# Optimization experiments

Hardware: AMD Instinct MI355X
Metric: run time of the kernel (lower is better)

## Reference

```python
import jax, jax.numpy as jnp
import numpy as np

# Standard genetic code, codons ordered by bases A<C<G<T (codon = b1*16 + b2*4 + b3)
GENETIC_CODE = "KNKNTTTTRSRSIIMIQHQHPPPPRRRRLLLLEDEDAAAAGGGGVVVV*Y*YSSSS*CWCLFLF"
V = 66  # codon vocab: 0 = pad, 1 = special, 2..65 = the 64 codons


def _tables():
    uniq = sorted(set(GENETIC_CODE))
    aa2g = {a: i for i, a in enumerate(uniq)}
    g_codon = np.array([aa2g[a] for a in GENETIC_CODE], np.int32)
    n_syn_g = np.bincount(g_codon, minlength=len(uniq))
    group_of_v = np.full(V, len(uniq), np.int32)  # pad/special -> dummy group
    group_of_v[2:] = g_codon
    n_syn_v = np.zeros(V, np.float32)
    n_syn_v[2:] = n_syn_g[g_codon]
    return jnp.asarray(group_of_v), jnp.asarray(n_syn_v), len(uniq) + 1

GROUP_OF_V, N_SYN_V, N_GROUPS = _tables()


def _cai(codon_ids, species_ids, mask, weight_matrix):
    # gather per-token CAI weight: [B,L]
    w = weight_matrix[species_ids[:, None], codon_ids]
    logw = jnp.log(jnp.clip(w, 1e-8))
    m = mask.astype(logw.dtype)
    mean_log = (logw * m).sum(1) / jnp.clip(m.sum(1), 1.0)
    return jnp.exp(mean_log)  # [B]


def _rscu_dist(codon_ids, mask):
    # per-sequence RSCU histogram: counts scattered per codon, normalized within
    # each synonymous-codon (amino-acid) group.
    B = codon_ids.shape[0]
    valid = (mask & (codon_ids >= 2)).astype(jnp.float32)  # real codons only
    b_idx = jnp.arange(B)[:, None]
    counts = jnp.zeros((B, V), jnp.float32).at[b_idx, codon_ids].add(valid)
    group_tot = jnp.zeros((B, N_GROUPS), jnp.float32).at[:, GROUP_OF_V].add(counts)
    denom = group_tot[:, GROUP_OF_V]  # [B,V]
    return jnp.where(denom > 0, counts * N_SYN_V / jnp.clip(denom, 1.0), 0.0)


def setup_inputs() -> dict:
    key = jax.random.key(0)
    ks = jax.random.split(key, 6)
    B, L = 128, 4096
    logits = jax.random.normal(ks[0], (B, L, V), jnp.float32)
    weight_matrix = jax.random.uniform(ks[1], (5, V), jnp.float32, 0.01, 1.0)
    ref_distributions = jax.random.uniform(ks[2], (5, V), jnp.float32, 0.0, 2.0)
    target_codon_ids = jax.random.randint(ks[3], (B, L), 0, V)
    aa_ids = jax.random.randint(ks[4], (B, L), 0, 24)
    species_ids = jax.random.randint(ks[5], (B,), 0, 5)
    mask = jnp.ones((B, L), bool)
    return {"logits": logits, "weight_matrix": weight_matrix,
            "ref_distributions": ref_distributions,
            "target_codon_ids": target_codon_ids, "aa_ids": aa_ids,
            "species_ids": species_ids, "mask": mask}


def reference(logits, weight_matrix, ref_distributions, target_codon_ids,
              aa_ids, species_ids, mask):
    pred = jnp.argmax(logits, -1)  # [B,L]
    # --- cross entropy with ignore_index=0 ---
    logp = jax.nn.log_softmax(logits, -1)
    nll = -jnp.take_along_axis(logp, target_codon_ids[..., None], -1)[..., 0]
    tvalid = (target_codon_ids != 0).astype(logits.dtype)
    ce = (nll * tvalid).sum() / jnp.clip(tvalid.sum(), 1.0)
    # --- CAI hinge loss ---
    pred_cai = _cai(pred, species_ids, mask, weight_matrix)
    tgt_cai = _cai(target_codon_ids, species_ids, mask, weight_matrix)
    cai_loss = jax.nn.relu(tgt_cai - pred_cai).mean()
    # --- RSCU KL divergence ---
    pred_rscu = _rscu_dist(pred, mask)
    tgt_rscu = _rscu_dist(target_codon_ids, mask)
    ref_rscu = ref_distributions[species_ids]  # [B,V]
    combined = 0.7 * tgt_rscu + 0.3 * ref_rscu + 1e-8
    p = pred_rscu + 1e-8
    p = p / p.sum(1, keepdims=True)
    t = combined / combined.sum(1, keepdims=True)
    rscu_loss = (t * jnp.log(t / p)).sum(1).mean()
    # gc/structure/dynamics (no features) and truncated rare_codon /
    # manufacturability terms contribute 0
    total = 1.0 * ce + 0.4 * cai_loss + 0.3 * rscu_loss
    return total
```

## Files before the change

kernel.cpp:

```cpp
#include <hip/hip_runtime.h>
#include <cstdint>
#include <cstddef>

__device__ static const int   d_GOV[66] = {
  21,21, 9,12, 9,12,17,17,17,17,15,16,15,16, 8, 8,11, 8,14, 7,14, 7,
  13,13,13,13,15,15,15,15,10,10,10,10, 4, 3, 4, 3, 1, 1, 1, 1, 6, 6,
   6, 6,18,18,18,18, 0,20, 0,20,16,16,16,16, 0, 2,19, 2,10, 5,10, 5};
__device__ static const float d_NSYN[66] = {
  0,0, 2,2,2,2, 4,4,4,4, 6,6,6,6, 3,3,1,3, 2,2,2,2, 4,4,4,4,
  6,6,6,6, 6,6,6,6, 2,2,2,2, 4,4,4,4, 4,4,4,4, 4,4,4,4,
  3,2,3,2, 6,6,6,6, 3,2,1,2, 6,2,6,2};


__global__ __launch_bounds__(128) void k_pos(
    const float* __restrict__ logits,
    const float* __restrict__ W,
    const int* __restrict__ tgt,
    const int* __restrict__ species,
    const unsigned char* __restrict__ mask,
    float* __restrict__ ws,
    int B, int L)
{
  const int tid  = threadIdx.x;
  const int lane = tid & 63;
  const int blk  = blockIdx.x;
  const int bpr  = L >> 9;
  const int b    = blk / bpr;
  const size_t base = (size_t)blk * 512;

  __shared__ __align__(16) float sT[128 * 66];
  __shared__ float s_logw[66];
  __shared__ int   s_cnt[132];
  __shared__ float s_acc[5];

  if (tid < 66)  s_logw[tid] = __logf(fmaxf(W[species[b] * 66 + tid], 1e-8f));
  s_cnt[tid] = 0;
  if (tid < 4)  s_cnt[128 + tid] = 0;
  if (tid < 5)  s_acc[tid] = 0.0f;

  const float2* g2 = reinterpret_cast<const float2*>(logits + base * 66);

  float2 r[33];
  #pragma unroll
  for (int i = 0; i < 33; ++i) r[i] = g2[i * 128 + tid];
  int   tg = tgt[base + tid];
  float mk = mask[base + tid] ? 1.0f : 0.0f;

  float acc0 = 0.f, acc1 = 0.f, acc2 = 0.f, acc3 = 0.f, acc4 = 0.f;

  #pragma unroll 1
  for (int c = 0; c < 4; ++c) {
    float2* s2 = reinterpret_cast<float2*>(sT);
    #pragma unroll
    for (int i = 0; i < 33; ++i) s2[i * 128 + tid] = r[i];
    __syncthreads();

    const int tgc = tg;  const float mkc = mk;

    if (c < 3) {
      const float2* gn = g2 + (size_t)(c + 1) * 4224;
      #pragma unroll
      for (int i = 0; i < 33; ++i) r[i] = gn[i * 128 + tid];
      tg = tgt[base + (size_t)(c + 1) * 128 + tid];
      mk = mask[base + (size_t)(c + 1) * 128 + tid] ? 1.0f : 0.0f;
    }
    __builtin_amdgcn_sched_barrier(0);

    const float2* row = reinterpret_cast<const float2*>(sT + tid * 66);
    float mx = -3.4e38f; int pr = 0;
    float seA = 0.f, seB = 0.f, xt = 0.f;
    #pragma unroll
    for (int j = 0; j < 33; ++j) {
      const float2 t = row[j];
      if (t.x > mx) { mx = t.x; pr = 2 * j; }
      if (t.y > mx) { mx = t.y; pr = 2 * j + 1; }
      seA += __expf(t.x);
      seB += __expf(t.y);
      if (2 * j     == tgc) xt = t.x;
      if (2 * j + 1 == tgc) xt = t.y;
    }
    const float nll = __logf(seA + seB) - xt;
    if (tgc != 0) { acc0 += nll; acc1 += 1.0f; }
    acc2 += s_logw[pr]  * mkc;
    acc3 += s_logw[tgc] * mkc;
    acc4 += mkc;
    if (mkc != 0.0f) {
      if (pr >= 2)  atomicAdd(&s_cnt[pr], 1);
      if (tgc >= 2) atomicAdd(&s_cnt[66 + tgc], 1);
    }
    __syncthreads();
  }

  #pragma unroll
  for (int off = 32; off > 0; off >>= 1) {
    acc0 += __shfl_xor(acc0, off);
    acc1 += __shfl_xor(acc1, off);
    acc2 += __shfl_xor(acc2, off);
    acc3 += __shfl_xor(acc3, off);
    acc4 += __shfl_xor(acc4, off);
  }
  if (lane == 0) {
    atomicAdd(&s_acc[0], acc0);
    atomicAdd(&s_acc[1], acc1);
    atomicAdd(&s_acc[2], acc2);
    atomicAdd(&s_acc[3], acc3);
    atomicAdd(&s_acc[4], acc4);
  }
  __syncthreads();

  int* wsi = (int*)ws;
  const int off_cp = 5 * B, off_ct = 5 * B + 66 * B;
  if (tid == 0) {
    atomicAdd(&ws[        b], s_acc[0]);
    atomicAdd(&ws[    B + b], s_acc[1]);
    atomicAdd(&ws[2 * B + b], s_acc[2]);
    atomicAdd(&ws[3 * B + b], s_acc[3]);
    atomicAdd(&ws[4 * B + b], s_acc[4]);
  }
  for (int j = tid; j < 132; j += 128) {
    const int cc = s_cnt[j];
    if (cc) {
      if (j < 66) atomicAdd(&wsi[off_cp + b * 66 + j], cc);
      else        atomicAdd(&wsi[off_ct + b * 66 + (j - 66)], cc);
    }
  }
}

__global__ __launch_bounds__(128) void k_row(
    const float* __restrict__ refd,
    const int* __restrict__ species,
    float* __restrict__ ws,
    int B)
{
  const int b    = blockIdx.x;
  const int tid  = threadIdx.x;
  const int lane = tid & 63;
  const int wave = tid >> 6;
  const int off_slp = 2 * B, off_slt = 3 * B, off_mc = 4 * B, off_cp = 5 * B;
  const int off_ct = 5 * B + 66 * B;
  const int off_res = 5 * B + 132 * B;
  const int* wsi = (const int*)ws;

  __shared__ float gp[24], gt[24];
  __shared__ float red[8];
  if (tid < 24) { gp[tid] = 0.0f; gt[tid] = 0.0f; }
  __syncthreads();

  float cp = 0.0f, ct = 0.0f, nsyn = 0.0f, ref = 0.0f;
  int gov = 22;
  if (tid < 66) {
    cp = (float)wsi[off_cp + b * 66 + tid];
    ct = (float)wsi[off_ct + b * 66 + tid];
    gov  = d_GOV[tid];
    nsyn = d_NSYN[tid];
    ref  = refd[species[b] * 66 + tid];
    atomicAdd(&gp[gov], cp);
    atomicAdd(&gt[gov], ct);
  }
  __syncthreads();

  float rp = 0.0f, rt = 0.0f;
  if (tid < 66) {
    float g1 = gp[gov]; rp = (g1 > 0.0f) ? cp * nsyn / g1 : 0.0f;
    float g2 = gt[gov]; rt = (g2 > 0.0f) ? ct * nsyn / g2 : 0.0f;
  }
  float pp = (tid < 66) ? (rp + 1e-8f) : 0.0f;
  float tp = (tid < 66) ? (0.7f * rt + 0.3f * ref + 1e-8f) : 0.0f;
  #pragma unroll
  for (int off = 32; off > 0; off >>= 1) {
    pp += __shfl_xor(pp, off);
    tp += __shfl_xor(tp, off);
  }
  if (lane == 0) { red[wave * 2] = pp; red[wave * 2 + 1] = tp; }
  __syncthreads();
  const float psum = red[0] + red[2];
  const float tsum = red[1] + red[3];

  float kl = 0.0f;
  if (tid < 66) {
    float pv = (rp + 1e-8f) / psum;
    float tv = (0.7f * rt + 0.3f * ref + 1e-8f) / tsum;
    kl = tv * __logf(tv / pv);
  }
  #pragma unroll
  for (int off = 32; off > 0; off >>= 1) kl += __shfl_xor(kl, off);
  if (lane == 0) red[4 + wave] = kl;
  __syncthreads();

  if (tid == 0) {
    float klt = red[4] + red[5];
    float mc    = fmaxf(ws[off_mc + b], 1.0f);
    float cai_p = __expf(ws[off_slp + b] / mc);
    float cai_t = __expf(ws[off_slt + b] / mc);
    float cai_l = fmaxf(cai_t - cai_p, 0.0f);
    ws[off_res + b] = 0.4f * cai_l + 0.3f * klt;
  }
}

__global__ __launch_bounds__(128) void k_sum(
    const float* __restrict__ ws,
    float* __restrict__ out, int B)
{
  const int t = threadIdx.x;
  const int lane = t & 63, wave = t >> 6;
  const int off_res = 5 * B + 132 * B;
  float cen = 0.f, ced = 0.f, res = 0.f;
  if (t < B) {
    cen = ws[t];
    ced = ws[B + t];
    res = ws[off_res + t];
  }
  #pragma unroll
  for (int off = 32; off > 0; off >>= 1) {
    cen += __shfl_xor(cen, off);
    ced += __shfl_xor(ced, off);
    res += __shfl_xor(res, off);
  }
  __shared__ float sr[6];
  if (lane == 0) { sr[wave * 3] = cen; sr[wave * 3 + 1] = ced; sr[wave * 3 + 2] = res; }
  __syncthreads();
  if (t == 0) {
    float n = sr[0] + sr[3], d = sr[1] + sr[4], r = sr[2] + sr[5];
    out[0] = n / fmaxf(d, 1.0f) + r / (float)B;
  }
}

extern "C" void kernel_launch(void* const* d_in, const int* in_sizes, int n_in,
                              void* d_out, int out_size, void* d_ws, size_t ws_size,
                              hipStream_t stream) {
  const float* logits  = (const float*)d_in[0];
  const float* W       = (const float*)d_in[1];
  const float* refd    = (const float*)d_in[2];
  const int*   tgt     = (const int*)d_in[3];
  const int*   species = (const int*)d_in[5];
  const unsigned char* mask = (const unsigned char*)d_in[6];
  float* out = (float*)d_out;
  float* ws  = (float*)d_ws;

  const int B = in_sizes[5];
  const int L = in_sizes[3] / B;
  const int nblk = (B * L) >> 9;

  const int ws_words = 6 * B + 132 * B;
  hipMemsetAsync(d_ws, 0, (size_t)ws_words * 4, stream);

  hipLaunchKernelGGL(k_pos, dim3(nblk), dim3(128), 0, stream,
                     logits, W, tgt, species, mask, ws, B, L);
  hipLaunchKernelGGL(k_row, dim3(B), dim3(128), 0, stream,
                     refd, species, ws, B);
  hipLaunchKernelGGL(k_sum, dim3(1), dim3(128), 0, stream,
                     ws, out, B);
}
```

Measured before the change: 42.77 us.

## Replace global atomics with per-block partials and fuse final reduction kernels

```diff
diff --git a/kernel.cpp b/kernel.cpp
--- a/kernel.cpp
+++ b/kernel.cpp
@@ -19,7 +19,7 @@
     const int* __restrict__ species,
     const unsigned char* __restrict__ mask,
     float* __restrict__ ws,
-    int B, int L)
+    int B, int L, int nblk)
 {
   const int tid  = threadIdx.x;
   const int lane = tid & 63;
@@ -38,11 +38,12 @@
   if (tid < 4)  s_cnt[128 + tid] = 0;
   if (tid < 5)  s_acc[tid] = 0.0f;
 
-  const float2* g2 = reinterpret_cast<const float2*>(logits + base * 66);
-
-  float2 r[33];
-  #pragma unroll
-  for (int i = 0; i < 33; ++i) r[i] = g2[i * 128 + tid];
+  const float4* g4 = reinterpret_cast<const float4*>(logits + base * 66);
+
+  float4 r[16]; float4 rtail;
+  #pragma unroll
+  for (int i = 0; i < 16; ++i) r[i] = g4[i * 128 + tid];
+  if (tid < 64) rtail = g4[2048 + tid];
   int   tg = tgt[base + tid];
   float mk = mask[base + tid] ? 1.0f : 0.0f;
 
@@ -50,17 +51,19 @@
 
   #pragma unroll 1
   for (int c = 0; c < 4; ++c) {
-    float2* s2 = reinterpret_cast<float2*>(sT);
-    #pragma unroll
-    for (int i = 0; i < 33; ++i) s2[i * 128 + tid] = r[i];
+    float4* s4 = reinterpret_cast<float4*>(sT);
+    #pragma unroll
+    for (int i = 0; i < 16; ++i) s4[i * 128 + tid] = r[i];
+    if (tid < 64) s4[2048 + tid] = rtail;
     __syncthreads();
 
     const int tgc = tg;  const float mkc = mk;
 
     if (c < 3) {
-      const float2* gn = g2 + (size_t)(c + 1) * 4224;
+      const float4* gn = g4 + (size_t)(c + 1) * 2112;
       #pragma unroll
-      for (int i = 0; i < 33; ++i) r[i] = gn[i * 128 + tid];
+      for (int i = 0; i < 16; ++i) r[i] = gn[i * 128 + tid];
+      if (tid < 64) rtail = gn[2048 + tid];
       tg = tgt[base + (size_t)(c + 1) * 128 + tid];
       mk = mask[base + (size_t)(c + 1) * 128 + tid] ? 1.0f : 0.0f;
     }
@@ -108,49 +111,48 @@
   }
   __syncthreads();
 
-  int* wsi = (int*)ws;
-  const int off_cp = 5 * B, off_ct = 5 * B + 66 * B;
-  if (tid == 0) {
-    atomicAdd(&ws[        b], s_acc[0]);
-    atomicAdd(&ws[    B + b], s_acc[1]);
-    atomicAdd(&ws[2 * B + b], s_acc[2]);
-    atomicAdd(&ws[3 * B + b], s_acc[3]);
-    atomicAdd(&ws[4 * B + b], s_acc[4]);
-  }
-  for (int j = tid; j < 132; j += 128) {
-    const int cc = s_cnt[j];
-    if (cc) {
-      if (j < 66) atomicAdd(&wsi[off_cp + b * 66 + j], cc);
-      else        atomicAdd(&wsi[off_ct + b * 66 + (j - 66)], cc);
-    }
-  }
+  float* wp = ws + (size_t)blk * 72;
+  if (tid < 5) wp[tid] = s_acc[tid];
+  if (tid < 66) {
+    unsigned h = (unsigned)s_cnt[tid] | ((unsigned)s_cnt[66 + tid] << 16);
+    reinterpret_cast<unsigned*>(wp)[5 + tid] = h;
+  }
+  if (blk == 0 && tid == 0)
+    reinterpret_cast<int*>(ws)[72 * nblk + 3 * B] = 0;
 }
 
-__global__ __launch_bounds__(128) void k_row(
+__global__ __launch_bounds__(128) void k_fin(
     const float* __restrict__ refd,
     const int* __restrict__ species,
     float* __restrict__ ws,
-    int B)
+    float* __restrict__ out,
+    int B, int nblk)
 {
   const int b    = blockIdx.x;
   const int tid  = threadIdx.x;
   const int lane = tid & 63;
   const int wave = tid >> 6;
-  const int off_slp = 2 * B, off_slt = 3 * B, off_mc = 4 * B, off_cp = 5 * B;
-  const int off_ct = 5 * B + 66 * B;
-  const int off_res = 5 * B + 132 * B;
-  const int* wsi = (const int*)ws;
+  const int bpb  = nblk / B;
+  const size_t off_row = (size_t)72 * nblk;
+  const size_t off_cnt = off_row + 3 * B;
+  const unsigned* wsu = reinterpret_cast<const unsigned*>(ws);
 
   __shared__ float gp[24], gt[24];
   __shared__ float red[8];
+  __shared__ float sp[5][8];
+  __shared__ int   s_last;
   if (tid < 24) { gp[tid] = 0.0f; gt[tid] = 0.0f; }
+  if (tid < 40) sp[tid % 5][tid / 5] = ws[(size_t)(b * bpb + tid / 5) * 72 + (tid % 5)];
   __syncthreads();
 
   float cp = 0.0f, ct = 0.0f, nsyn = 0.0f, ref = 0.0f;
   int gov = 22;
   if (tid < 66) {
-    cp = (float)wsi[off_cp + b * 66 + tid];
-    ct = (float)wsi[off_ct + b * 66 + tid];
+    for (int k = 0; k < bpb; ++k) {
+      const unsigned h = wsu[(size_t)(b * bpb + k) * 72 + 5 + tid];
+      cp += (float)(h & 0xffffu);
+      ct += (float)(h >> 16);
+    }
     gov  = d_GOV[tid];
     nsyn = d_NSYN[tid];
     ref  = refd[species[b] * 66 + tid];
@@ -189,39 +191,42 @@
 
   if (tid == 0) {
     float klt = red[4] + red[5];
-    float mc    = fmaxf(ws[off_mc + b], 1.0f);
-    float cai_p = __expf(ws[off_slp + b] / mc);
-    float cai_t = __expf(ws[off_slt + b] / mc);
-    float cai_l = fmaxf(cai_t - cai_p, 0.0f);
-    ws[off_res + b] = 0.4f * cai_l + 0.3f * klt;
-  }
-}
-
-__global__ __launch_bounds__(128) void k_sum(
-    const float* __restrict__ ws,
-    float* __restrict__ out, int B)
-{
-  const int t = threadIdx.x;
-  const int lane = t & 63, wave = t >> 6;
-  const int off_res = 5 * B + 132 * B;
-  float cen = 0.f, ced = 0.f, res = 0.f;
-  if (t < B) {
-    cen = ws[t];
-    ced = ws[B + t];
-    res = ws[off_res + t];
-  }
-  #pragma unroll
-  for (int off = 32; off > 0; off >>= 1) {
-    cen += __shfl_xor(cen, off);
-    ced += __shfl_xor(ced, off);
-    res += __shfl_xor(res, off);
-  }
-  __shared__ float sr[6];
-  if (lane == 0) { sr[wave * 3] = cen; sr[wave * 3 + 1] = ced; sr[wave * 3 + 2] = res; }
-  __syncthreads();
-  if (t == 0) {
-    float n = sr[0] + sr[3], d = sr[1] + sr[4], r = sr[2] + sr[5];
-    out[0] = n / fmaxf(d, 1.0f) + r / (float)B;
+    float cen = 0.f, ced = 0.f, slp = 0.f, slt = 0.f, mc = 0.f;
+    #pragma unroll
+    for (int k = 0; k < 8; ++k) {
+      cen += sp[0][k]; ced += sp[1][k]; slp += sp[2][k]; slt += sp[3][k]; mc += sp[4][k];
+    }
+    mc = fmaxf(mc, 1.0f);
+    const float cai_l = fmaxf(__expf(slt / mc) - __expf(slp / mc), 0.0f);
+    float* rowp = ws + off_row + (size_t)b * 3;
+    rowp[0] = cen;
+    rowp[1] = ced;
+    rowp[2] = 0.4f * cai_l + 0.3f * klt;
+  }
+
+  __threadfence();
+  if (tid == 0) s_last = atomicAdd(reinterpret_cast<int*>(ws) + off_cnt, 1);
+  __syncthreads();
+  if (s_last == B - 1) {
+    __threadfence();
+    float cen = 0.f, ced = 0.f, res = 0.f;
+    if (tid < B) {
+      const float* rowp = ws + off_row + (size_t)tid * 3;
+      cen = rowp[0]; ced = rowp[1]; res = rowp[2];
+    }
+    #pragma unroll
+    for (int off = 32; off > 0; off >>= 1) {
+      cen += __shfl_xor(cen, off);
+      ced += __shfl_xor(ced, off);
+      res += __shfl_xor(res, off);
+    }
+    __shared__ float sr[6];
+    if (lane == 0) { sr[wave * 3] = cen; sr[wave * 3 + 1] = ced; sr[wave * 3 + 2] = res; }
+    __syncthreads();
+    if (tid == 0) {
+      float n = sr[0] + sr[3], d = sr[1] + sr[4], rsum = sr[2] + sr[5];
+      out[0] = n / fmaxf(d, 1.0f) + rsum / (float)B;
+    }
   }
 }
 
@@ -241,13 +246,8 @@
   const int L = in_sizes[3] / B;
   const int nblk = (B * L) >> 9;
 
-  const int ws_words = 6 * B + 132 * B;
-  hipMemsetAsync(d_ws, 0, (size_t)ws_words * 4, stream);
-
   hipLaunchKernelGGL(k_pos, dim3(nblk), dim3(128), 0, stream,
-                     logits, W, tgt, species, mask, ws, B, L);
-  hipLaunchKernelGGL(k_row, dim3(B), dim3(128), 0, stream,
-                     refd, species, ws, B);
-  hipLaunchKernelGGL(k_sum, dim3(1), dim3(128), 0, stream,
-                     ws, out, B);
+                     logits, W, tgt, species, mask, ws, B, L, nblk);
+  hipLaunchKernelGGL(k_fin, dim3(B), dim3(128), 0, stream,
+                     refd, species, ws, out, B, nblk);
 }
```

After: 77.94 us. +82.2%, slower.
